# Optimization experiments

Measured on AMD Instinct MI355X. Metric: run time of the kernel, lower is better.

Reference implementation:

```python
import jax, jax.numpy as jnp
import numpy as np

B, N, IN_DIM, OUT = 4, 4096, 3, 40
NPTS = [1024, 256, 64, 16]   # base_points // sampling_ratio
K, FIRST_K = 8, 16
EPS = 1e-5

def gelu(t):
    return jax.nn.gelu(t, approximate=False)  # torch nn.GELU default (erf)

def pdist2(a, b):
    # a: (b,d,m), b: (b,d,n) -> squared pairwise distances (b,m,n)
    aa = jnp.sum(a * a, axis=1)[:, :, None]
    bb = jnp.sum(b * b, axis=1)[:, None, :]
    return aa + bb - 2.0 * jnp.einsum('bdm,bdn->bmn', a, b)

def knn_idx(a, b, k):
    # indices of k nearest points of b for each point of a
    return jax.lax.top_k(-pdist2(a, b), k)[1]

def gather_nbr(x, ind):
    # x: (b,d,n), ind: (b,m,k) -> (b,d,m,k)
    b, d, n = x.shape
    m, k = ind.shape[1], ind.shape[2]
    idx = jnp.broadcast_to(ind.reshape(b, 1, m * k), (b, d, m * k))
    return jnp.take_along_axis(x, idx, axis=2).reshape(b, d, m, k)

def bn(x):
    # BatchNorm (training-mode batch stats, gamma=1, beta=0 as at init)
    ax = (0,) + tuple(range(2, x.ndim))
    mu = jnp.mean(x, axis=ax, keepdims=True)
    var = jnp.mean((x - mu) ** 2, axis=ax, keepdims=True)
    return (x - mu) / jnp.sqrt(var + EPS)

def route(x, nbr):
    # (b,d,n),(b,n,k) -> (b,2d,n,k) : cat([neighbor - center, center])
    sel = gather_nbr(x, nbr)
    xc = x[:, :, :, None]
    return jnp.concatenate([sel - xc, jnp.broadcast_to(xc, sel.shape)], axis=1)

def edge_conv(x, l1, l2, sc, k, nbr=None):
    if nbr is None:
        nbr = knn_idx(x, x, k)  # dynamic graph in feature space
    h = jnp.max(jnp.einsum('of,bfnk->bonk', l1, route(x, nbr)), axis=-1)
    h = gelu(bn(h))
    h = jnp.max(jnp.einsum('of,bfnk->bonk', l2, route(h, nbr)), axis=-1)
    short = x if sc is None else jnp.einsum('of,bfn->bon', sc, x)
    return gelu(bn(short + h))

def fps(xyz, m):
    # farthest point sampling; xyz: (b,3,n) -> indices (b,m); start index 0
    pts = jnp.transpose(xyz, (0, 2, 1))  # (b,n,3)
    b, n, _ = pts.shape
    def body(carry, _):
        dmin, last = carry
        lp = jnp.take_along_axis(pts, last[:, None, None], axis=1)  # (b,1,3)
        d = jnp.sum((pts - lp) ** 2, axis=-1)
        dmin = jnp.minimum(dmin, d)
        nxt = jnp.argmax(dmin, axis=-1).astype(jnp.int32)
        return (dmin, nxt), last
    init = (jnp.full((b, n), jnp.inf, pts.dtype), jnp.zeros((b,), jnp.int32))
    _, inds = jax.lax.scan(body, init, None, length=m)
    return jnp.transpose(inds)  # (b,m)

def _forward(x, xyz, mlp_w, mlp_b, c0_l1, c0_l2, l1s, l2s, scs,
             head_w1, head_w2, head_b2):
    b = x.shape[0]
    nbr0 = knn_idx(xyz, xyz, FIRST_K)
    h = gelu(bn(jnp.einsum('oi,bin->bon', mlp_w, x) + mlp_b[None, :, None]))
    h = edge_conv(h, c0_l1, c0_l2, None, FIRST_K, nbr=nbr0)
    cur = xyz
    for i in range(4):
        m = NPTS[i]
        sind = fps(cur, m)
        sxyz = jnp.take_along_axis(
            cur, jnp.broadcast_to(sind[:, None, :], (b, cur.shape[1], m)), axis=2)
        nbr = knn_idx(sxyz, cur, K)
        cur = jnp.mean(gather_nbr(cur, nbr), axis=-1)      # sampled xyz = nbr mean
        h = jnp.max(gather_nbr(h, nbr), axis=-1)           # sampled feat = nbr max
        h = edge_conv(h, l1s[i], l2s[i], scs[i], K)
    g = jnp.mean(h, axis=-1)                               # global average pool
    g = gelu(bn(g @ head_w1.T))
    return g @ head_w2.T + head_b2[None, :]


def setup_inputs() -> dict:
    key = jax.random.key(0)
    ks = jax.random.split(key, 20)
    def w(k, o, i):
        return (jax.random.normal(k, (o, i), jnp.float32) / np.sqrt(i)).astype(jnp.float32)
    return {
        'x': jax.random.normal(ks[0], (B, IN_DIM, N), jnp.float32),
        'xyz': jax.random.normal(ks[1], (B, 3, N), jnp.float32),
        'mlp_w': w(ks[2], 64, IN_DIM), 'mlp_b': jnp.zeros((64,), jnp.float32),
        'c0_l1': w(ks[3], 64, 128), 'c0_l2': w(ks[4], 64, 128),
        's0_l1': w(ks[5], 64, 128), 's0_l2': w(ks[6], 64, 128),
        's1_l1': w(ks[7], 128, 128), 's1_l2': w(ks[8], 128, 256), 's1_sc': w(ks[9], 128, 64),
        's2_l1': w(ks[10], 256, 256), 's2_l2': w(ks[11], 256, 512), 's2_sc': w(ks[12], 256, 128),
        's3_l1': w(ks[13], 512, 512), 's3_l2': w(ks[14], 512, 1024), 's3_sc': w(ks[15], 512, 256),
        'head_w1': w(ks[16], 256, 512), 'head_w2': w(ks[17], OUT, 256),
        'head_b2': jnp.zeros((OUT,), jnp.float32),
    }


def reference(x, xyz, mlp_w, mlp_b, c0_l1, c0_l2, s0_l1, s0_l2,
              s1_l1, s1_l2, s1_sc, s2_l1, s2_l2, s2_sc, s3_l1, s3_l2, s3_sc,
              head_w1, head_w2, head_b2):
    return _forward(x, xyz, mlp_w, mlp_b, c0_l1, c0_l2,
                    (s0_l1, s1_l1, s2_l1, s3_l1),
                    (s0_l2, s1_l2, s2_l2, s3_l2),
                    (None, s1_sc, s2_sc, s3_sc),
                    head_w1, head_w2, head_b2)
```

## Files before the change

kernel.cpp:

```cpp
#include <hip/hip_runtime.h>
#include <math.h>

#define NCHUNK 32
typedef unsigned long long ull;

__device__ __forceinline__ float gelu_f(float v){
  return 0.5f*v*(1.0f+erff(v*0.70710678118654752440f));
}

__device__ __forceinline__ unsigned flipf(float d){
  unsigned u = __float_as_uint(d);
  return (u & 0x80000000u) ? ~u : (u | 0x80000000u);
}

template<int CTRL>
__device__ __forceinline__ ull dpp64(ull k){
  int lo = __builtin_amdgcn_update_dpp(0, (int)(unsigned)k,       CTRL, 0xF, 0xF, true);
  int hi = __builtin_amdgcn_update_dpp(0, (int)(unsigned)(k>>32), CTRL, 0xF, 0xF, true);
  return ((ull)(unsigned)hi<<32) | (unsigned)lo;
}
__device__ __forceinline__ ull rl64(ull k, int l){
  unsigned lo = (unsigned)__builtin_amdgcn_readlane((int)(unsigned)k, l);
  unsigned hi = (unsigned)__builtin_amdgcn_readlane((int)(unsigned)(k>>32), l);
  return ((ull)hi<<32) | lo;
}
__device__ __forceinline__ ull fmax64(ull a, ull b){
  return (ull)__double_as_longlong(fmax(__longlong_as_double((long long)a),
                                        __longlong_as_double((long long)b)));
}
__device__ __forceinline__ ull wave_fmax(ull k){
  k = fmax64(k, dpp64<0xB1>(k));
  k = fmax64(k, dpp64<0x4E>(k));
  k = fmax64(k, dpp64<0x141>(k));
  k = fmax64(k, dpp64<0x140>(k));
  ull a=rl64(k,0), b=rl64(k,16), c=rl64(k,32), d=rl64(k,48);
  return fmax64(fmax64(a,b), fmax64(c,d));
}
template<int CTRL>
__device__ __forceinline__ ull kmin_dpp(ull k){
  ull o = dpp64<CTRL>(k);
  return o < k ? o : k;
}
__device__ __forceinline__ ull wave_kmin(ull k){
  k = kmin_dpp<0xB1>(k);
  k = kmin_dpp<0x4E>(k);
  k = kmin_dpp<0x141>(k);
  k = kmin_dpp<0x140>(k);
  ull a=rl64(k,0), b=rl64(k,16), c=rl64(k,32), d=rl64(k,48);
  ull ab = a < b ? a : b, cd = c < d ? c : d;
  return ab < cd ? ab : cd;
}


template<int K, int T>
__device__ __forceinline__ void knn_body(
    const float* __restrict__ cand, int n,
    const float* __restrict__ qsrc, const int* __restrict__ qidx, int m,
    int* __restrict__ nbr, float* __restrict__ outc,
    int b, int qblk, int qoff, char* smem)
{
  float4* tile = (float4*)smem;
  constexpr int NWV = T/64;
  int wv = threadIdx.x >> 6, lane = threadIdx.x & 63;
  int q = qblk*NWV + wv + qoff;
  const float* cb = cand + (size_t)b*3*n;
  int qi = qidx ? qidx[(size_t)b*m + q] : q;
  const float* qb = qsrc + (size_t)b*3*n;
  float qx = qb[qi], qy = qb[n+qi], qz = qb[2*n+qi];
  float aa = (qx*qx + qy*qy) + qz*qz;

  ull a[K];
  #pragma unroll
  for (int k=0;k<K;k++) a[k] = ~0ull;
  ull worst = ~0ull; int wslot = 0;

  for (int base=0; base<n; base+=1024){
    int cnt = min(1024, n-base);
    for (int j=threadIdx.x; j<cnt; j+=T){
      float x=cb[base+j], y=cb[n+base+j], z=cb[2*n+base+j];
      tile[j] = make_float4(x,y,z,(x*x+y*y)+z*z);
    }
    __syncthreads();
    int steps = cnt >> 6;
    for (int i=0;i<steps;i++){
      int j = lane + (i<<6);
      float4 c = tile[j];
      float d = aa + c.w - 2.0f*((qx*c.x+qy*c.y)+qz*c.z);
      ull key = ((ull)flipf(d)<<32) | (unsigned)(base+j);
      if (key < worst){
        #pragma unroll
        for (int k=0;k<K;k++) if (k==wslot) a[k] = key;
        worst = a[0]; wslot = 0;
        #pragma unroll
        for (int k=1;k<K;k++){
          bool g = a[k] > worst;
          worst = g ? a[k] : worst;
          wslot = g ? k : wslot;
        }
      }
    }
    __syncthreads();
  }

  #pragma unroll
  for (int kk=2; kk<=K; kk<<=1)
    #pragma unroll
    for (int jj=kk>>1; jj>0; jj>>=1)
      #pragma unroll
      for (int i=0;i<K;i++){
        int l = i ^ jj;
        if (l > i){
          bool dirUp = ((i & kk) == 0);
          ull x = a[i], y = a[l];
          bool sw = dirUp ? (x > y) : (x < y);
          a[i] = sw ? y : x;
          a[l] = sw ? x : y;
        }
      }

  ull head = a[0];
  int res[K];
  #pragma unroll
  for (int r=0; r<K; r++){
    ull mk = wave_kmin(head);
    res[r] = (int)(unsigned)mk;
    if (head == mk){
      #pragma unroll
      for (int i2=0;i2<K-1;i2++) a[i2]=a[i2+1];
      a[K-1] = ~0ull;
      head = a[0];
    }
  }
  if (lane == 0){
    int* o = nbr + ((size_t)b*m + q)*K;
    #pragma unroll
    for (int r=0;r<K;r++) o[r] = res[r];
  }
  if (outc != nullptr && lane < 3){
    const float* cd = cb + (size_t)lane*n;
    float s=0;
    #pragma unroll
    for (int k=0;k<K;k++) s += cd[res[k]];
    outc[((size_t)b*3 + lane)*m + q] = s * (1.0f/K);
  }
}

template<int NP, int T, int M>
__device__ __forceinline__ void fps_mw_seg(const float* __restrict__ cur, int n,
                                           int* __restrict__ sind, float* __restrict__ gdmin,
                                           int b, int M0, int M1, char* smem)
{
  constexpr int NW = T/64;
  int tid = threadIdx.x;
  int wv = tid>>6;
  const float* cb = cur + (size_t)b*3*n;
  float4* lp = (float4*)smem;
  ull* wred = (ull*)(smem + sizeof(float4)*NP*T);
  float* gd = gdmin + (size_t)b*n;
  float px[NP], py[NP], pz[NP], dmin[NP];
  unsigned nj[NP];
  #pragma unroll
  for (int s=0;s<NP;s++){
    int j = tid + s*T;
    px[s]=cb[j]; py[s]=cb[n+j]; pz[s]=cb[2*n+j];
    dmin[s] = (M0==0) ? 1e30f : gd[j];
    nj[s] = (unsigned)(~j);
    lp[j] = make_float4(px[s],py[s],pz[s],0.f);
  }
  __syncthreads();
  int ci = (M0==0) ? 0 : sind[(size_t)b*M + (M0-1)];
  float4 w0 = lp[ci];
  float X = w0.x, Y = w0.y, Z = w0.z;
  if (M0==0 && tid==0) sind[(size_t)b*M] = 0;
  __builtin_amdgcn_s_setprio(3);
  int p = 0;
  int s0 = (M0==0) ? 1 : M0;
  for (int step=s0; step<M1; step++){
    ull key[NP];
    #pragma unroll
    for (int s=0;s<NP;s++){
      float dx=px[s]-X, dy=py[s]-Y, dz=pz[s]-Z;
      float d = (dx*dx + dy*dy) + dz*dz;
      float nd = fminf(dmin[s], d);
      dmin[s] = nd;
      key[s] = ((ull)__float_as_uint(nd)<<32) | nj[s];
    }
    #pragma unroll
    for (int w=NP; w>1; w>>=1)
      #pragma unroll
      for (int i=0;i<NP;i++) if (i < (w>>1))
        key[i] = fmax64(key[i], key[i+(w>>1)]);
    ull wk = wave_fmax(key[0]);
    if ((tid&63)==0) wred[p*NW + wv] = wk;
    __syncthreads();
    const ulonglong2* wp2 = (const ulonglong2*)(wred + p*NW);
    ulonglong2 m0 = wp2[0], m1 = wp2[1], m2 = wp2[2], m3 = wp2[3];
    ull gk = fmax64(fmax64(fmax64(m0.x,m0.y), fmax64(m1.x,m1.y)),
                    fmax64(fmax64(m2.x,m2.y), fmax64(m3.x,m3.y)));
    int gi = (int)(~(unsigned)gk);
    if (tid==0) sind[(size_t)b*M + step] = gi;
    float4 wp = lp[gi];
    X=wp.x; Y=wp.y; Z=wp.z;
    p ^= 1;
  }
  __builtin_amdgcn_s_setprio(0);
  #pragma unroll
  for (int s=0;s<NP;s++) gd[tid + s*T] = dmin[s];
}

template<int NP, int M>
__device__ __forceinline__ void fps_sw_body(const float* __restrict__ cur, int n,
                                            int* __restrict__ sind, int b, char* smem)
{
  int lane = threadIdx.x;
  const float* cb = cur + (size_t)b*3*n;
  float4* lp = (float4*)smem;
  float px[NP], py[NP], pz[NP], dmin[NP];
  unsigned nj[NP];
  #pragma unroll
  for (int s=0;s<NP;s++){
    int j = lane + s*64;
    px[s]=cb[j]; py[s]=cb[n+j]; pz[s]=cb[2*n+j]; dmin[s]=1e30f;
    nj[s] = (unsigned)(~j);
    lp[j] = make_float4(px[s],py[s],pz[s],0.f);
  }
  float X = lp[0].x, Y = lp[0].y, Z = lp[0].z;
  if (lane==0) sind[(size_t)b*M] = 0;
  __builtin_amdgcn_s_setprio(3);
  for (int step=1; step<M; step++){
    ull key[NP];
    #pragma unroll
    for (int s=0;s<NP;s++){
      float dx=px[s]-X, dy=py[s]-Y, dz=pz[s]-Z;
      float d = (dx*dx + dy*dy) + dz*dz;
      float nd = fminf(dmin[s], d);
      dmin[s] = nd;
      key[s] = ((ull)__float_as_uint(nd)<<32) | nj[s];
    }
    #pragma unroll
    for (int w=NP; w>1; w>>=1)
      #pragma unroll
      for (int i=0;i<NP;i++) if (i < (w>>1))
        key[i] = fmax64(key[i], key[i+(w>>1)]);
    ull gk = wave_fmax(key[0]);
    int gi = (int)(~(unsigned)gk);
    if (lane==0) sind[(size_t)b*M + step] = gi;
    float4 wp = lp[gi];
    X=wp.x; Y=wp.y; Z=wp.z;
  }
  __builtin_amdgcn_s_setprio(0);
}

template<bool DUAL, bool BN>
__device__ __forceinline__ void gemm_body(
    const float* __restrict__ A, const float* __restrict__ B,
    float* __restrict__ out0, float* __restrict__ out1,
    int M, int N, int Kd, int lda, int ldb, int ldo, int boff,
    long sA, long sB, long sO, const float* __restrict__ part, float invR,
    int bxi, int byi, int bzi, char* smem)
{
  A += (size_t)bzi * sA; B += (size_t)bzi * sB;
  float* o0 = out0 + (size_t)bzi * sO;
  float* o1 = DUAL ? (out1 + (size_t)bzi * sO) : nullptr;
  int rowBase = byi*64, colBase = bxi*64;
  float (*As)[64]  = (float(*)[64])smem;
  float (*Bs0)[64] = (float(*)[64])(smem + 4096);
  float (*Bs1)[64] = (float(*)[64])(smem + 8192);
  float* mu_s = (float*)(smem + 12288);
  float* var_s = mu_s + 512;
  int tid = threadIdx.x;
  if (BN){
    for (int oo=tid; oo<Kd; oo+=blockDim.x){
      float s=0, q=0;
      #pragma unroll 4
      for (int c=0;c<NCHUNK;c++){
        s += part[(size_t)c*1024 + oo];
        q += part[(size_t)(NCHUNK+c)*1024 + oo];
      }
      float mu = s*invR;
      mu_s[oo] = mu;
      var_s[oo] = q*invR - mu*mu;
    }
    __syncthreads();
  }
  int ty = tid>>4, tx = tid&15;
  float acc0[4][4] = {}, acc1[4][4] = {};
  int lr = tid>>2, lk = (tid&3)*4;
  for (int k0=0; k0<Kd; k0+=16) {
    float4 va = make_float4(0,0,0,0);
    int r = rowBase + lr;
    if (r < M) va = *(const float4*)(A + (size_t)r*lda + k0 + lk);
    if (BN){
      int c = k0 + lk;
      va.x = gelu_f((va.x - mu_s[c+0]) / sqrtf(var_s[c+0] + 1e-5f));
      va.y = gelu_f((va.y - mu_s[c+1]) / sqrtf(var_s[c+1] + 1e-5f));
      va.z = gelu_f((va.z - mu_s[c+2]) / sqrtf(var_s[c+2] + 1e-5f));
      va.w = gelu_f((va.w - mu_s[c+3]) / sqrtf(var_s[c+3] + 1e-5f));
    }
    As[lk+0][lr]=va.x; As[lk+1][lr]=va.y; As[lk+2][lr]=va.z; As[lk+3][lr]=va.w;
    float4 vb = make_float4(0,0,0,0), vb2 = make_float4(0,0,0,0);
    int c2 = colBase + lr;
    if (c2 < N) {
      vb = *(const float4*)(B + (size_t)c2*ldb + k0 + lk);
      if (DUAL) vb2 = *(const float4*)(B + (size_t)c2*ldb + boff + k0 + lk);
    }
    Bs0[lk+0][lr]=vb.x; Bs0[lk+1][lr]=vb.y; Bs0[lk+2][lr]=vb.z; Bs0[lk+3][lr]=vb.w;
    if (DUAL) {
      Bs1[lk+0][lr]=vb2.x-vb.x; Bs1[lk+1][lr]=vb2.y-vb.y;
      Bs1[lk+2][lr]=vb2.z-vb.z; Bs1[lk+3][lr]=vb2.w-vb.w;
    }
    __syncthreads();
    #pragma unroll
    for (int kk=0;kk<16;kk++){
      float4 a  = *(const float4*)&As[kk][ty*4];
      float4 b0 = *(const float4*)&Bs0[kk][tx*4];
      float av[4]={a.x,a.y,a.z,a.w};
      float b0v[4]={b0.x,b0.y,b0.z,b0.w};
      #pragma unroll
      for (int i=0;i<4;i++)
        #pragma unroll
        for (int j=0;j<4;j++) acc0[i][j] = fmaf(av[i], b0v[j], acc0[i][j]);
      if (DUAL) {
        float4 b1 = *(const float4*)&Bs1[kk][tx*4];
        float b1v[4]={b1.x,b1.y,b1.z,b1.w};
        #pragma unroll
        for (int i=0;i<4;i++)
          #pragma unroll
          for (int j=0;j<4;j++) acc1[i][j] = fmaf(av[i], b1v[j], acc1[i][j]);
      }
    }
    __syncthreads();
  }
  #pragma unroll
  for (int i=0;i<4;i++){
    int r = rowBase + ty*4 + i;
    if (r < M) {
      #pragma unroll
      for (int j=0;j<4;j++){
        int c = colBase + tx*4 + j;
        if (c < N) {
          o0[(size_t)r*ldo + c] = acc0[i][j];
          if (DUAL) o1[(size_t)r*ldo + c] = acc1[i][j];
        }
      }
    }
  }
}

template<bool DUAL, bool BN>
__device__ __forceinline__ void gemm_body_g(
    const float* __restrict__ A, const float* __restrict__ B,
    float* __restrict__ out0, float* __restrict__ out1,
    int M, int N, int Kd, int lda, int ldb, int ldo, int boff,
    const float* __restrict__ part, float invR,
    int bxi, int byi, char* smem)
{
  int rowBase = byi*64, colBase = bxi*64;
  float (*As)[64]  = (float(*)[64])smem;
  float (*Bs0)[64] = (float(*)[64])(smem + 4096);
  float (*Bs1)[64] = (float(*)[64])(smem + 8192);
  float* mu_s = (float*)(smem + 12288);
  float* var_s = mu_s + 512;
  int tid = threadIdx.x;
  bool act = tid < 256;
  if (BN){
    for (int oo=tid; oo<Kd; oo+=blockDim.x){
      float s=0, q=0;
      #pragma unroll 4
      for (int c=0;c<NCHUNK;c++){
        s += part[(size_t)c*1024 + oo];
        q += part[(size_t)(NCHUNK+c)*1024 + oo];
      }
      float mu = s*invR;
      mu_s[oo] = mu;
      var_s[oo] = q*invR - mu*mu;
    }
    __syncthreads();
  }
  int ty = tid>>4, tx = tid&15;
  float acc0[4][4] = {}, acc1[4][4] = {};
  int lr = tid>>2, lk = (tid&3)*4;
  for (int k0=0; k0<Kd; k0+=16) {
    if (act){
      float4 va = make_float4(0,0,0,0);
      int r = rowBase + lr;
      if (r < M) va = *(const float4*)(A + (size_t)r*lda + k0 + lk);
      if (BN){
        int c = k0 + lk;
        va.x = gelu_f((va.x - mu_s[c+0]) / sqrtf(var_s[c+0] + 1e-5f));
        va.y = gelu_f((va.y - mu_s[c+1]) / sqrtf(var_s[c+1] + 1e-5f));
        va.z = gelu_f((va.z - mu_s[c+2]) / sqrtf(var_s[c+2] + 1e-5f));
        va.w = gelu_f((va.w - mu_s[c+3]) / sqrtf(var_s[c+3] + 1e-5f));
      }
      As[lk+0][lr]=va.x; As[lk+1][lr]=va.y; As[lk+2][lr]=va.z; As[lk+3][lr]=va.w;
      float4 vb = make_float4(0,0,0,0), vb2 = make_float4(0,0,0,0);
      int c2 = colBase + lr;
      if (c2 < N) {
        vb = *(const float4*)(B + (size_t)c2*ldb + k0 + lk);
        if (DUAL) vb2 = *(const float4*)(B + (size_t)c2*ldb + boff + k0 + lk);
      }
      Bs0[lk+0][lr]=vb.x; Bs0[lk+1][lr]=vb.y; Bs0[lk+2][lr]=vb.z; Bs0[lk+3][lr]=vb.w;
      if (DUAL) {
        Bs1[lk+0][lr]=vb2.x-vb.x; Bs1[lk+1][lr]=vb2.y-vb.y;
        Bs1[lk+2][lr]=vb2.z-vb.z; Bs1[lk+3][lr]=vb2.w-vb.w;
      }
    }
    __syncthreads();
    if (act){
      #pragma unroll
      for (int kk=0;kk<16;kk++){
        float4 a  = *(const float4*)&As[kk][ty*4];
        float4 b0 = *(const float4*)&Bs0[kk][tx*4];
        float av[4]={a.x,a.y,a.z,a.w};
        float b0v[4]={b0.x,b0.y,b0.z,b0.w};
        #pragma unroll
        for (int i=0;i<4;i++)
          #pragma unroll
          for (int j=0;j<4;j++) acc0[i][j] = fmaf(av[i], b0v[j], acc0[i][j]);
        if (DUAL) {
          float4 b1 = *(const float4*)&Bs1[kk][tx*4];
          float b1v[4]={b1.x,b1.y,b1.z,b1.w};
          #pragma unroll
          for (int i=0;i<4;i++)
            #pragma unroll
            for (int j=0;j<4;j++) acc1[i][j] = fmaf(av[i], b1v[j], acc1[i][j]);
        }
      }
    }
    __syncthreads();
  }
  if (act){
    #pragma unroll
    for (int i=0;i<4;i++){
      int r = rowBase + ty*4 + i;
      if (r < M) {
        #pragma unroll
        for (int j=0;j<4;j++){
          int c = colBase + tx*4 + j;
          if (c < N) {
            out0[(size_t)r*ldo + c] = acc0[i][j];
            if (DUAL) out1[(size_t)r*ldo + c] = acc1[i][j];
          }
        }
      }
    }
  }
}

__device__ __forceinline__ void gather_elem(
    const float* __restrict__ P, const int* __restrict__ nbr,
    const float* __restrict__ addA, const float* __restrict__ addB,
    float* __restrict__ out, int n_out, int n_src, int O, int K, int total, int e)
{
  if (e >= total) return;
  int o = e % O; int r = e / O;
  int b = r / n_out; int i = r % n_out;
  const int* nb = nbr + ((size_t)b*n_out + i)*K;
  float mx = -1e38f;
  for (int k=0;k<K;k++){
    int j = nb[k];
    float v = P[((size_t)b*n_src + j)*O + o];
    mx = fmaxf(mx, v);
  }
  float res = mx;
  if (addA) res += addA[e];
  if (addB) res = addB[e] + res;
  out[e] = res;
}

__device__ __forceinline__ void gatherbn_body(
    const float* __restrict__ P, const int* __restrict__ nbr,
    const float* __restrict__ part, float invR,
    float* __restrict__ out, float* __restrict__ aa,
    int n_out, int n_src, int O, int K, int blk, char* smem)
{
  float* mu_s = (float*)smem; float* var_s = mu_s + 256; float* sv = var_s + 256;
  int tid = threadIdx.x;
  for (int oo=tid; oo<O; oo+=256){
    float s=0, q=0;
    #pragma unroll 4
    for (int c=0;c<NCHUNK;c++){
      s += part[(size_t)c*1024 + oo];
      q += part[(size_t)(NCHUNK+c)*1024 + oo];
    }
    float mu = s*invR;
    mu_s[oo] = mu;
    var_s[oo] = q*invR - mu*mu;
  }
  __syncthreads();
  int e = blk*256 + tid;
  int o = e % O; int r = e / O;
  int b = r / n_out; int i = r % n_out;
  const int* nb = nbr + ((size_t)b*n_out + i)*K;
  float mu = mu_s[o], sd = sqrtf(var_s[o] + 1e-5f);
  float mx = -1e38f;
  for (int k=0;k<K;k++){
    int j = nb[k];
    float p = P[((size_t)b*n_src + j)*O + o];
    float v = gelu_f((p - mu)/sd);
    mx = fmaxf(mx, v);
  }
  out[e] = mx;
  sv[tid] = mx*mx;
  __syncthreads();
  for (int st=O>>1; st>0; st>>=1){
    if (o < st) sv[tid] += sv[tid+st];
    __syncthreads();
  }
  if (o == 0) aa[r] = sv[tid];
}


#define FPS_SMEM 65664

__global__ __launch_bounds__(512,2) void mega1(
    const float* __restrict__ xyz, const float* __restrict__ x,
    const float* __restrict__ mlpw, const float* __restrict__ mlpb,
    int* __restrict__ sind0, float* __restrict__ gdmin,
    int* __restrict__ nbr0, float* __restrict__ hA, int M0, int M1)
{
  __shared__ __align__(16) char SMEM[FPS_SMEM];
  int bid = blockIdx.x;
  if (bid < 4){
    fps_mw_seg<8,512,1024>(xyz, 4096, sind0, gdmin, bid, M0, M1, SMEM);
  } else if (bid < 4+2048){
    int kb = bid - 4;
    knn_body<16,512>(xyz, 4096, xyz, nullptr, 4096, nbr0, nullptr, kb>>9, kb&511, 0, SMEM);
  } else {
    int e = (bid - 2052)*512 + threadIdx.x;
    if (e < 4*4096*64){
      int o = e & 63; int r = e >> 6;
      int b = r / 4096; int i = r % 4096;
      const float* xb = x + (size_t)b*3*4096;
      hA[e] = ((mlpw[o*3+0]*xb[i] + mlpw[o*3+1]*xb[4096+i]) + mlpw[o*3+2]*xb[2*4096+i]) + mlpb[o];
    }
  }
}

__global__ __launch_bounds__(512,2) void fps_bngelu(
    const float* fcur, int* sind, float* gdmin, int M0, int M1,
    float* __restrict__ xx, const float* __restrict__ part, float invR, int O, int total)
{
  __shared__ __align__(16) char SMEM[FPS_SMEM];
  if (blockIdx.x < 4){
    fps_mw_seg<8,512,1024>(fcur, 4096, sind, gdmin, blockIdx.x, M0, M1, SMEM);
    return;
  }
  float* mu_s = (float*)SMEM; float* var_s = mu_s + 512;
  for (int oo=threadIdx.x; oo<O; oo+=512){
    float s=0, q=0;
    #pragma unroll 4
    for (int c=0;c<NCHUNK;c++){
      s += part[(size_t)c*1024 + oo];
      q += part[(size_t)(NCHUNK+c)*1024 + oo];
    }
    float mu = s*invR;
    mu_s[oo] = mu;
    var_s[oo] = q*invR - mu*mu;
  }
  __syncthreads();
  int e = (blockIdx.x-4)*512 + threadIdx.x;
  if (e >= total) return;
  int o = e % O;
  float v = (xx[e]-mu_s[o]) / sqrtf(var_s[o] + 1e-5f);
  xx[e] = gelu_f(v);
}

template<bool DUAL, bool BN>
__global__ __launch_bounds__(512,2) void fps0_gemm(
    const float* fcur, int* sind, float* gdmin, int M0, int M1,
    const float* A, const float* B, float* out0, float* out1,
    int Mg, int Ng, int Kd, int lda, int ldb, int ldo, int boff,
    const float* part, float invR, int nbx)
{
  __shared__ __align__(16) char SMEM[FPS_SMEM];
  if (blockIdx.x < 4){
    fps_mw_seg<8,512,1024>(fcur, 4096, sind, gdmin, blockIdx.x, M0, M1, SMEM);
    return;
  }
  int l = blockIdx.x - 4;
  gemm_body_g<DUAL,BN>(A,B,out0,out1,Mg,Ng,Kd,lda,ldb,ldo,boff,part,invR, l%nbx, l/nbx, SMEM);
}

__global__ __launch_bounds__(512,2) void fps0_gather_knn(
    const float* fcur, int* sind, float* gdmin, int M0, int M1,
    const float* cand, int n, const float* qsrc, const int* qidx, int m,
    int* nbrOut, float* outc, int KNB,
    const float* P, const int* nbr, const float* addA, const float* addB,
    float* out, int n_out, int n_src, int O, int K, int total)
{
  __shared__ __align__(16) char SMEM[FPS_SMEM];
  if (blockIdx.x < 4){
    fps_mw_seg<8,512,1024>(fcur, 4096, sind, gdmin, blockIdx.x, M0, M1, SMEM);
    return;
  }
  int l = blockIdx.x - 4;
  if (l < KNB){
    knn_body<8,512>(cand, n, qsrc, qidx, m, nbrOut, outc, l>>6, l&63, 0, SMEM);
    return;
  }
  int e = (l-KNB)*512 + threadIdx.x;
  gather_elem(P, nbr, addA, addB, out, n_out, n_src, O, K, total, e);
}

__global__ __launch_bounds__(512,2) void fps0_gather(
    const float* fcur, int* sind, float* gdmin, int M0, int M1,
    const float* P, const int* nbr, const float* addA, const float* addB,
    float* out, int n_out, int n_src, int O, int K, int total)
{
  __shared__ __align__(16) char SMEM[FPS_SMEM];
  if (blockIdx.x < 4){
    fps_mw_seg<8,512,1024>(fcur, 4096, sind, gdmin, blockIdx.x, M0, M1, SMEM);
    return;
  }
  int e = (blockIdx.x-4)*512 + threadIdx.x;
  gather_elem(P, nbr, addA, addB, out, n_out, n_src, O, K, total, e);
}

__global__ __launch_bounds__(512,2) void fps0_stats(
    const float* fcur, int* sind, float* gdmin, int M0, int M1,
    const float* __restrict__ x, int R, int O, float* __restrict__ part)
{
  __shared__ __align__(16) char SMEM[FPS_SMEM];
  if (blockIdx.x < 4){
    fps_mw_seg<8,512,1024>(fcur, 4096, sind, gdmin, blockIdx.x, M0, M1, SMEM);
    return;
  }
  int o = threadIdx.x;
  if (o >= O) return;
  int chunk = blockIdx.x - 4;
  int per = (R + NCHUNK - 1)/NCHUNK;
  int r0 = chunk*per, r1 = min(r0+per, R);
  float s=0, q=0;
  for (int r=r0; r<r1; r++){ float v = x[(size_t)r*O + o]; s+=v; q+=v*v; }
  part[(size_t)chunk*1024 + o] = s;
  part[(size_t)(NCHUNK+chunk)*1024 + o] = q;
}

__global__ __launch_bounds__(256) void knn_wave8(
    const float* cand, int n, const float* qsrc, const int* qidx, int m, int qoff,
    int* nbr, float* outc)
{
  __shared__ __align__(16) char SMEM[16384];
  knn_body<8,256>(cand, n, qsrc, qidx, m, nbr, outc, blockIdx.y, blockIdx.x, qoff, SMEM);
}

template<int NP, int M>
__global__ __launch_bounds__(256) void fps_gatherbn(
    const float* fcur, int fn, int* sind,
    const float* P, const int* nbr, const float* part, float invR,
    float* out, float* aa, int n_out, int n_src, int O, int K)
{
  __shared__ __align__(16) char SMEM[(NP*64*16 > 16384) ? NP*64*16 : 16384];
  if (blockIdx.x < 4){
    if (threadIdx.x < 64) fps_sw_body<NP,M>(fcur, fn, sind, blockIdx.x, SMEM);
    return;
  }
  gatherbn_body(P, nbr, part, invR, out, aa, n_out, n_src, O, K, blockIdx.x-4, SMEM);
}

template<int NP, int M, bool DUAL, bool BN>
__global__ __launch_bounds__(256) void fps_gemm(
    const float* fcur, int fn, int* sind,
    const float* A, const float* B, float* out0, float* out1,
    int Mg, int Ng, int Kd, int lda, int ldb, int ldo, int boff,
    const float* part, float invR, int nbx, int nby)
{
  __shared__ __align__(16) char SMEM[(NP*64*16 > 16896) ? NP*64*16 : 16896];
  if (blockIdx.x < 4){
    if (threadIdx.x < 64) fps_sw_body<NP,M>(fcur, fn, sind, blockIdx.x, SMEM);
    return;
  }
  int l = blockIdx.x - 4;
  int bx = l % nbx, by = (l/nbx) % nby, bz = l/(nbx*nby);
  gemm_body<DUAL,BN>(A,B,out0,out1,Mg,Ng,Kd,lda,ldb,ldo,boff,0,0,0,part,invR,bx,by,bz,SMEM);
}

__global__ __launch_bounds__(256) void knn_gather(
    const float* cand, int n, const float* qsrc, const int* qidx, int m,
    int* nbrOut, float* outc, int KNB,
    const float* P, const int* nbr, const float* addA, const float* addB,
    float* out, int n_out, int n_src, int O, int K, int total)
{
  __shared__ __align__(16) char SMEM[16384];
  if (blockIdx.x < KNB){
    int qpb = m/4;
    knn_body<8,256>(cand, n, qsrc, qidx, m, nbrOut, outc, blockIdx.x/qpb, blockIdx.x%qpb, 0, SMEM);
    return;
  }
  gather_elem(P, nbr, addA, addB, out, n_out, n_src, O, K, total, (blockIdx.x-KNB)*256 + threadIdx.x);
}

__global__ __launch_bounds__(256) void knn_gemm(
    const float* cand, int n, const float* qsrc, const int* qidx, int m,
    int* nbrOut, float* outc, int KNB,
    const float* A, const float* B, float* out0,
    int Mg, int Ng, int Kd, int lda, int ldb, int ldo,
    long sA, long sB, long sO, int nbx, int nby)
{
  __shared__ __align__(16) char SMEM[16896];
  if (blockIdx.x < KNB){
    int qpb = m/4;
    knn_body<8,256>(cand, n, qsrc, qidx, m, nbrOut, outc, blockIdx.x/qpb, blockIdx.x%qpb, 0, SMEM);
    return;
  }
  int l = blockIdx.x - KNB;
  int bx = l % nbx, by = (l/nbx) % nby, bz = l/(nbx*nby);
  gemm_body<false,false>(A,B,out0,nullptr,Mg,Ng,Kd,lda,ldb,ldo,0,sA,sB,sO,nullptr,0.f,bx,by,bz,SMEM);
}

template<bool DUAL, bool BN>
__global__ __launch_bounds__(256) void gemm_nt(
    const float* A, const float* B, float* out0, float* out1,
    int M, int N, int Kd, int lda, int ldb, int ldo, int boff,
    long sA, long sB, long sO, const float* part, float invR)
{
  __shared__ __align__(16) char SMEM[16896];
  gemm_body<DUAL,BN>(A,B,out0,out1,M,N,Kd,lda,ldb,ldo,boff,sA,sB,sO,part,invR,
                     blockIdx.x, blockIdx.y, blockIdx.z, SMEM);
}

__global__ __launch_bounds__(256) void gemm2sc(
    const float* A2, const float* B2, float* o20, float* o21, int R, int O2, int O1v,
    const float* part, float invR,
    const float* Asc, const float* Bsc, float* osc, int Cin,
    int nbx, int nby)
{
  __shared__ __align__(16) char SMEM[16896];
  int l = blockIdx.x;
  int half = nbx*nby;
  if (l < half){
    gemm_body<true,true>(A2,B2,o20,o21,R,O2,O1v,O1v,2*O1v,O2,O1v,0,0,0,part,invR, l%nbx, l/nbx, 0, SMEM);
  } else {
    l -= half;
    gemm_body<false,false>(Asc,Bsc,osc,nullptr,R,O2,Cin,Cin,Cin,O2,0,0,0,0,nullptr,0.f, l%nbx, l/nbx, 0, SMEM);
  }
}

__global__ __launch_bounds__(256) void gathermax_kernel(
    const float* P, const int* nbr, const float* addA, const float* addB,
    float* out, int n_out, int n_src, int O, int K, int total)
{
  gather_elem(P, nbr, addA, addB, out, n_out, n_src, O, K, total, blockIdx.x*256 + threadIdx.x);
}

__global__ __launch_bounds__(256) void gatherbn_kernel(
    const float* P, const int* nbr, const float* part, float invR,
    float* out, float* aa, int n_out, int n_src, int O, int K)
{
  __shared__ __align__(16) char SMEM[3072];
  gatherbn_body(P, nbr, part, invR, out, aa, n_out, n_src, O, K, blockIdx.x, SMEM);
}

template<int K>
__global__ __launch_bounds__(256) void topk_wave(
    const float* __restrict__ G, const float* __restrict__ aa, int m,
    int* __restrict__ nbr)
{
  __shared__ float abs_s[1024];
  int b = blockIdx.y;
  int wv = threadIdx.x >> 6, lane = threadIdx.x & 63;
  int q = blockIdx.x*4 + wv;
  const float* ab = aa + (size_t)b*m;
  for (int j=threadIdx.x; j<m; j+=256) abs_s[j] = ab[j];
  __syncthreads();
  float aq = ab[q];
  const float* Gq = G + ((size_t)b*m + q)*m;

  ull a[K];
  #pragma unroll
  for (int k=0;k<K;k++) a[k] = ~0ull;
  ull worst = ~0ull; int wslot = 0;

  int steps = (m+63)>>6;
  for (int i=0;i<steps;i++){
    int j = lane + (i<<6);
    ull key = ~0ull;
    if (j < m){
      float g = Gq[j];
      float d = aq + abs_s[j] - 2.0f*g;
      key = ((ull)flipf(d)<<32) | (unsigned)j;
    }
    if (key < worst){
      #pragma unroll
      for (int k=0;k<K;k++) if (k==wslot) a[k] = key;
      worst = a[0]; wslot = 0;
      #pragma unroll
      for (int k=1;k<K;k++){
        bool g = a[k] > worst;
        worst = g ? a[k] : worst;
        wslot = g ? k : wslot;
      }
    }
  }
  #pragma unroll
  for (int kk=2; kk<=K; kk<<=1)
    #pragma unroll
    for (int jj=kk>>1; jj>0; jj>>=1)
      #pragma unroll
      for (int i=0;i<K;i++){
        int l = i ^ jj;
        if (l > i){
          bool dirUp = ((i & kk) == 0);
          ull x = a[i], y = a[l];
          bool sw = dirUp ? (x > y) : (x < y);
          a[i] = sw ? y : x;
          a[l] = sw ? x : y;
        }
      }
  ull head = a[0];
  int res[K];
  #pragma unroll
  for (int r=0; r<K; r++){
    ull mk = wave_kmin(head);
    res[r] = (int)(unsigned)mk;
    if (head == mk){
      #pragma unroll
      for (int i2=0;i2<K-1;i2++) a[i2]=a[i2+1];
      a[K-1] = ~0ull;
      head = a[0];
    }
  }
  if (lane == 0){
    int* o = nbr + ((size_t)b*m + q)*K;
    #pragma unroll
    for (int r=0;r<K;r++) o[r] = res[r];
  }
}

__global__ void stats_part_kernel(const float* __restrict__ x, int R, int O,
                                  float* __restrict__ part)
{
  int o = threadIdx.x;
  int chunk = blockIdx.x;
  int per = (R + NCHUNK - 1)/NCHUNK;
  int r0 = chunk*per, r1 = min(r0+per, R);
  float s=0, q=0;
  for (int r=r0; r<r1; r++){ float v = x[(size_t)r*O + o]; s+=v; q+=v*v; }
  part[(size_t)chunk*1024 + o] = s;
  part[(size_t)(NCHUNK+chunk)*1024 + o] = q;
}

__global__ __launch_bounds__(1024) void head_kernel(const float* __restrict__ h,
    const float* __restrict__ part, float invR,
    const float* __restrict__ w1, const float* __restrict__ w2,
    const float* __restrict__ b2, float* __restrict__ out)
{
  __shared__ __align__(16) float mu_s[512], var_s[512];
  __shared__ __align__(16) float g[4*512];
  __shared__ __align__(16) float t[4*256];
  int tid = threadIdx.x;
  for (int oo=tid; oo<512; oo+=1024){
    float s=0, q=0;
    #pragma unroll 4
    for (int c=0;c<NCHUNK;c++){
      s += part[(size_t)c*1024 + oo];
      q += part[(size_t)(NCHUNK+c)*1024 + oo];
    }
    float mu = s*invR;
    mu_s[oo] = mu;
    var_s[oo] = q*invR - mu*mu;
  }
  __syncthreads();
  for (int e=tid; e<2048; e+=1024){
    int b=e>>9, c=e&511;
    float mu = mu_s[c], sd = sqrtf(var_s[c] + 1e-5f);
    float s=0;
    for (int p=0;p<16;p++){
      float v = h[((size_t)(b*16+p))*512 + c];
      s += gelu_f((v-mu)/sd);
    }
    g[e] = s * (1.0f/16.0f);
  }
  __syncthreads();
  {
    int b = tid>>8, j = tid&255;
    const float4* gr = (const float4*)(g + b*512);
    const float4* wr = (const float4*)(w1 + (size_t)j*512);
    float s=0;
    for (int c=0;c<128;c++){
      float4 a=gr[c], w=wr[c];
      s = fmaf(a.x,w.x, fmaf(a.y,w.y, fmaf(a.z,w.z, fmaf(a.w,w.w, s))));
    }
    t[tid] = s;
  }
  __syncthreads();
  if (tid < 256){
    float v0=t[tid], v1=t[256+tid], v2=t[512+tid], v3=t[768+tid];
    float mu = ((v0+v1)+v2+v3)*0.25f;
    float d0=v0-mu, d1=v1-mu, d2=v2-mu, d3=v3-mu;
    float var = ((d0*d0+d1*d1)+d2*d2+d3*d3)*0.25f;
    float sq = sqrtf(var + 1e-5f);
    t[tid]     = gelu_f(d0/sq);
    t[256+tid] = gelu_f(d1/sq);
    t[512+tid] = gelu_f(d2/sq);
    t[768+tid] = gelu_f(d3/sq);
  }
  __syncthreads();
  if (tid < 160){
    int b = tid/40, o = tid%40;
    const float* tr = t + b*256; const float* wr = w2 + (size_t)o*256;
    float s=0;
    for (int j=0;j<256;j++) s = fmaf(tr[j], wr[j], s);
    out[tid] = s + b2[o];
  }
}

extern "C" void kernel_launch(void* const* d_in, const int* in_sizes, int n_in,
                              void* d_out, int out_size, void* d_ws, size_t ws_size,
                              hipStream_t stream)
{
  const float* x    = (const float*)d_in[0];
  const float* xyz  = (const float*)d_in[1];
  const float* mlpw = (const float*)d_in[2];
  const float* mlpb = (const float*)d_in[3];
  const float* c0l1 = (const float*)d_in[4];
  const float* c0l2 = (const float*)d_in[5];
  const float* L1[4] = {(const float*)d_in[6], (const float*)d_in[8],
                        (const float*)d_in[11], (const float*)d_in[14]};
  const float* L2[4] = {(const float*)d_in[7], (const float*)d_in[9],
                        (const float*)d_in[12], (const float*)d_in[15]};
  const float* SC[4] = {nullptr, (const float*)d_in[10],
                        (const float*)d_in[13], (const float*)d_in[16]};
  const float* hw1 = (const float*)d_in[17];
  const float* hw2 = (const float*)d_in[18];
  const float* hb2 = (const float*)d_in[19];
  float* out = (float*)d_out;

  float* ws = (float*)d_ws;
  const size_t MF = 1024*1024;
  float* D    = ws;
  float* hA   = ws + 4*MF;
  float* hX   = ws + 5*MF;
  float* hP   = ws + 6*MF;
  float* hCT  = ws + 7*MF;
  float* hSH  = ws + 8*MF;
  float* hH1  = ws + 9*MF;
  float* hOUT = ws + 10*MF;
  float* aux  = ws + 11*MF;
  int*   nbr0  = (int*)aux;                 aux += 262144;
  int*   nbrS0 = (int*)aux;                 aux += 32768;
  int*   nbrS1 = (int*)aux;                 aux += 8192;
  int*   nbrS2 = (int*)aux;                 aux += 2048;
  int*   nbrS3 = (int*)aux;                 aux += 512;
  int*   nbrF  = (int*)aux;                 aux += 32768;
  int*   sind0 = (int*)aux;                 aux += 4096;
  int*   sind1 = (int*)aux;                 aux += 1024;
  int*   sind2 = (int*)aux;                 aux += 256;
  int*   sind3 = (int*)aux;                 aux += 64;
  float* aa    = aux;                       aux += 4096;
  float* cur1  = aux;                       aux += 12288;
  float* cur2  = aux;                       aux += 3072;
  float* cur3  = aux;                       aux += 768;
  float* part  = aux;                       aux += 65536;
  float* gdmin = aux;                       aux += 16384;

  int tot0 = 4*4096*64;

  mega1<<<4100, 512, 0, stream>>>(xyz, x, mlpw, mlpb, sind0, gdmin, nbr0, hA, 0, 260);
  stats_part_kernel<<<NCHUNK, 64, 0, stream>>>(hA, 16384, 64, part);
  fps_bngelu<<<4+2048, 512, 0, stream>>>(xyz, sind0, gdmin, 260, 390, hA, part, 1.0f/16384.0f, 64, tot0);
  fps0_gemm<true,false><<<4+256, 512, 0, stream>>>(xyz, sind0, gdmin, 390, 517,
      hA, c0l1, hP, hCT, 16384, 64, 64, 64, 128, 64, 64, nullptr, 0.f, 1);
  fps0_gather_knn<<<4+256+2048, 512, 0, stream>>>(xyz, sind0, gdmin, 517, 644,
      xyz, 4096, xyz, sind0, 1024, nbrS0, cur1, 256,
      hP, nbr0, hCT, nullptr, hH1, 4096, 4096, 64, 16, 1048576);
  stats_part_kernel<<<NCHUNK, 64, 0, stream>>>(hH1, 16384, 64, part);
  fps0_gemm<true,true><<<4+256, 512, 0, stream>>>(xyz, sind0, gdmin, 644, 771,
      hH1, c0l2, hP, hCT, 16384, 64, 64, 64, 128, 64, 64, part, 1.0f/16384.0f, 1);
  fps0_gather<<<4+2048, 512, 0, stream>>>(xyz, sind0, gdmin, 771, 898,
      hP, nbr0, hCT, hA, hOUT, 4096, 4096, 64, 16, 1048576);
  fps0_stats<<<4+NCHUNK, 512, 0, stream>>>(xyz, sind0, gdmin, 898, 1024,
      hOUT, 16384, 64, part);

  knn_wave8<<<dim3(128,4),256,0,stream>>>(xyz, 4096, xyz, sind0, 1024, 512, nbrS0, cur1);

  fps_gatherbn<16,256><<<4+1024,256,0,stream>>>(cur1, 1024, sind1,
      hOUT, nbrS0, part, 1.0f/16384.0f, hX, aa, 1024, 4096, 64, 8);
  knn_gemm<<<256+1024,256,0,stream>>>(cur1, 1024, cur1, sind1, 256, nbrS1, cur2, 256,
      hX, hX, D, 1024, 1024, 64, 64, 64, 1024,
      (long)1024*64, (long)1024*64, (long)1024*1024, 16, 16);
  topk_wave<8><<<dim3(256,4),256,0,stream>>>(D, aa, 1024, nbrF);
  fps_gemm<4,64,true,false><<<4+64,256,0,stream>>>(cur2, 256, sind2,
      hX, L1[0], hP, hCT, 4096, 64, 64, 64, 128, 64, 64, nullptr, 0.f, 1, 64);
  knn_gather<<<64+1024,256,0,stream>>>(cur2, 256, cur2, sind2, 64, nbrS2, cur3, 64,
      hP, nbrF, hCT, nullptr, hH1, 1024, 1024, 64, 8, 262144);
  stats_part_kernel<<<NCHUNK, 64, 0, stream>>>(hH1, 4096, 64, part);
  fps_gemm<1,16,true,true><<<4+64,256,0,stream>>>(cur3, 64, sind3,
      hH1, L2[0], hP, hCT, 4096, 64, 64, 64, 128, 64, 64, part, 1.0f/4096.0f, 1, 64);
  knn_gather<<<16+1024,256,0,stream>>>(cur3, 64, cur3, sind3, 16, nbrS3, nullptr, 16,
      hP, nbrF, hCT, hX, hA, 1024, 1024, 64, 8, 262144);
  stats_part_kernel<<<NCHUNK, 64, 0, stream>>>(hA, 4096, 64, part);

  const int   mArr[3]   = {256, 64, 16};
  const int   nsrcArr[3]= {1024, 256, 64};
  const int   CinArr[3] = {64, 128, 256};
  const int   OArr[3]   = {128, 256, 512};
  const int*  nbrSs[3]  = {nbrS1, nbrS2, nbrS3};
  float* hcur = hA;
  float invRprev = 1.0f/4096.0f;
  for (int s=0;s<3;s++){
    int m = mArr[s], nsrc = nsrcArr[s], Cin = CinArr[s], O1 = OArr[s], O2 = OArr[s];
    int R = 4*m;
    int th = R*Cin;
    gatherbn_kernel<<<th/256,256,0,stream>>>(hcur, nbrSs[s], part, invRprev,
                                             hX, aa, m, nsrc, Cin, 8);
    dim3 gp((m+63)/64, (m+63)/64, 4);
    gemm_nt<false,false><<<gp,256,0,stream>>>(hX, hX, D, nullptr, m, m, Cin, Cin, Cin, m, 0,
                                              (long)m*Cin, (long)m*Cin, (long)m*m, nullptr, 0.f);
    topk_wave<8><<<dim3(m/4,4),256,0,stream>>>(D, aa, m, nbrF);
    dim3 gg1((O1+63)/64, (R+63)/64, 1);
    gemm_nt<true,false><<<gg1,256,0,stream>>>(hX, L1[s+1], hP, hCT, R, O1, Cin, Cin, 2*Cin, O1, Cin, 0,0,0, nullptr, 0.f);
    int t1 = R*O1;
    gathermax_kernel<<<(t1+255)/256,256,0,stream>>>(hP, nbrF, hCT, nullptr, hH1, m, m, O1, 8, t1);
    stats_part_kernel<<<NCHUNK, O1, 0, stream>>>(hH1, R, O1, part);
    int nbx = (O2+63)/64, nby = (R+63)/64;
    gemm2sc<<<2*nbx*nby,256,0,stream>>>(hH1, L2[s+1], hP, hCT, R, O2, O1, part, 1.0f/R,
                                        hX, SC[s+1], hSH, Cin, nbx, nby);
    int t2 = R*O2;
    float* outbuf = (s&1) ? hA : hOUT;
    gathermax_kernel<<<(t2+255)/256,256,0,stream>>>(hP, nbrF, hCT, hSH, outbuf, m, m, O2, 8, t2);
    stats_part_kernel<<<NCHUNK, O2, 0, stream>>>(outbuf, R, O2, part);
    hcur = outbuf;
    invRprev = 1.0f/R;
  }

  head_kernel<<<1,1024,0,stream>>>(hcur, part, 1.0f/64.0f, hw1, hw2, hb2, out);
}
```

Before: 1.755 ms.

## Carry argmax coordinates through FPS reduction instead of staging all points in LDS

The farthest-point-sampling segment no longer copies all 4096 point coordinates into shared memory. Each wave writes the coordinates of its winning point alongside its key, and the block-level reduction now tracks which wave won so the next centre is read from that small slot. This removes a 64 KB LDS footprint from every fused kernel that shares the FPS code, so the co-scheduled gemm, knn, gather and stats blocks can run at higher occupancy. It also drops the initial staging barrier. In exchange each step does an extra per-wave coordinate write and a serial compare chain.

Result: slower. 1.949 ms (+11.0%).

```diff
diff --git a/kernel.cpp b/kernel.cpp
--- a/kernel.cpp
+++ b/kernel.cpp
@@ -154,8 +154,8 @@
   int tid = threadIdx.x;
   int wv = tid>>6;
   const float* cb = cur + (size_t)b*3*n;
-  float4* lp = (float4*)smem;
-  ull* wred = (ull*)(smem + sizeof(float4)*NP*T);
+  ull*    wred   = (ull*)smem;
+  float4* wcoord = (float4*)(smem + 2*NW*8);
   float* gd = gdmin + (size_t)b*n;
   float px[NP], py[NP], pz[NP], dmin[NP];
   unsigned nj[NP];
@@ -165,12 +165,9 @@
     px[s]=cb[j]; py[s]=cb[n+j]; pz[s]=cb[2*n+j];
     dmin[s] = (M0==0) ? 1e30f : gd[j];
     nj[s] = (unsigned)(~j);
-    lp[j] = make_float4(px[s],py[s],pz[s],0.f);
-  }
-  __syncthreads();
+  }
   int ci = (M0==0) ? 0 : sind[(size_t)b*M + (M0-1)];
-  float4 w0 = lp[ci];
-  float X = w0.x, Y = w0.y, Z = w0.z;
+  float X = cb[ci], Y = cb[n+ci], Z = cb[2*n+ci];
   if (M0==0 && tid==0) sind[(size_t)b*M] = 0;
   __builtin_amdgcn_s_setprio(3);
   int p = 0;
@@ -191,15 +188,24 @@
       for (int i=0;i<NP;i++) if (i < (w>>1))
         key[i] = fmax64(key[i], key[i+(w>>1)]);
     ull wk = wave_fmax(key[0]);
+    #pragma unroll
+    for (int s=0;s<NP;s++)
+      if (nj[s] == (unsigned)wk) wcoord[p*NW + wv] = make_float4(px[s],py[s],pz[s],0.f);
     if ((tid&63)==0) wred[p*NW + wv] = wk;
     __syncthreads();
     const ulonglong2* wp2 = (const ulonglong2*)(wred + p*NW);
     ulonglong2 m0 = wp2[0], m1 = wp2[1], m2 = wp2[2], m3 = wp2[3];
-    ull gk = fmax64(fmax64(fmax64(m0.x,m0.y), fmax64(m1.x,m1.y)),
-                    fmax64(fmax64(m2.x,m2.y), fmax64(m3.x,m3.y)));
+    ull gk = m0.x; int wvm = 0;
+    if (m0.y > gk){ gk=m0.y; wvm=1; }
+    if (m1.x > gk){ gk=m1.x; wvm=2; }
+    if (m1.y > gk){ gk=m1.y; wvm=3; }
+    if (m2.x > gk){ gk=m2.x; wvm=4; }
+    if (m2.y > gk){ gk=m2.y; wvm=5; }
+    if (m3.x > gk){ gk=m3.x; wvm=6; }
+    if (m3.y > gk){ gk=m3.y; wvm=7; }
     int gi = (int)(~(unsigned)gk);
     if (tid==0) sind[(size_t)b*M + step] = gi;
-    float4 wp = lp[gi];
+    float4 wp = wcoord[p*NW + wvm];
     X=wp.x; Y=wp.y; Z=wp.z;
     p ^= 1;
   }
@@ -511,15 +517,13 @@
 }
 
 
-#define FPS_SMEM 65664
-
 __global__ __launch_bounds__(512,2) void mega1(
     const float* __restrict__ xyz, const float* __restrict__ x,
     const float* __restrict__ mlpw, const float* __restrict__ mlpb,
     int* __restrict__ sind0, float* __restrict__ gdmin,
     int* __restrict__ nbr0, float* __restrict__ hA, int M0, int M1)
 {
-  __shared__ __align__(16) char SMEM[FPS_SMEM];
+  __shared__ __align__(16) char SMEM[16384];
   int bid = blockIdx.x;
   if (bid < 4){
     fps_mw_seg<8,512,1024>(xyz, 4096, sind0, gdmin, bid, M0, M1, SMEM);
@@ -541,7 +545,7 @@
     const float* fcur, int* sind, float* gdmin, int M0, int M1,
     float* __restrict__ xx, const float* __restrict__ part, float invR, int O, int total)
 {
-  __shared__ __align__(16) char SMEM[FPS_SMEM];
+  __shared__ __align__(16) char SMEM[4096];
   if (blockIdx.x < 4){
     fps_mw_seg<8,512,1024>(fcur, 4096, sind, gdmin, blockIdx.x, M0, M1, SMEM);
     return;
@@ -573,7 +577,7 @@
     int Mg, int Ng, int Kd, int lda, int ldb, int ldo, int boff,
     const float* part, float invR, int nbx)
 {
-  __shared__ __align__(16) char SMEM[FPS_SMEM];
+  __shared__ __align__(16) char SMEM[16896];
   if (blockIdx.x < 4){
     fps_mw_seg<8,512,1024>(fcur, 4096, sind, gdmin, blockIdx.x, M0, M1, SMEM);
     return;
@@ -589,7 +593,7 @@
     const float* P, const int* nbr, const float* addA, const float* addB,
     float* out, int n_out, int n_src, int O, int K, int total)
 {
-  __shared__ __align__(16) char SMEM[FPS_SMEM];
+  __shared__ __align__(16) char SMEM[16384];
   if (blockIdx.x < 4){
     fps_mw_seg<8,512,1024>(fcur, 4096, sind, gdmin, blockIdx.x, M0, M1, SMEM);
     return;
@@ -608,7 +612,7 @@
     const float* P, const int* nbr, const float* addA, const float* addB,
     float* out, int n_out, int n_src, int O, int K, int total)
 {
-  __shared__ __align__(16) char SMEM[FPS_SMEM];
+  __shared__ __align__(16) char SMEM[512];
   if (blockIdx.x < 4){
     fps_mw_seg<8,512,1024>(fcur, 4096, sind, gdmin, blockIdx.x, M0, M1, SMEM);
     return;
@@ -621,7 +625,7 @@
     const float* fcur, int* sind, float* gdmin, int M0, int M1,
     const float* __restrict__ x, int R, int O, float* __restrict__ part)
 {
-  __shared__ __align__(16) char SMEM[FPS_SMEM];
+  __shared__ __align__(16) char SMEM[512];
   if (blockIdx.x < 4){
     fps_mw_seg<8,512,1024>(fcur, 4096, sind, gdmin, blockIdx.x, M0, M1, SMEM);
     return;
```
